# Optimization experiments

Hardware: AMD Instinct MI355X
Metric: run time of the kernel (lower is better)

## Reference

```python
import jax, jax.numpy as jnp
import numpy as np

NUM_USERS = 100000
NUM_ITEMS = 100000
EMBED_F = 64
BATCH = 8192
MAX_HIST = 200
MU = 3.5


def setup_inputs() -> dict:
    key = jax.random.key(0)
    ks = jax.random.split(key, 9)
    inv_f = 1.0 / EMBED_F
    return {
        "user": jax.random.randint(ks[0], (BATCH,), 0, NUM_USERS),
        "item": jax.random.randint(ks[1], (BATCH,), 0, NUM_ITEMS),
        "implicit": jax.random.randint(ks[2], (BATCH, MAX_HIST), 0, NUM_ITEMS),
        "hist_len": jax.random.randint(ks[3], (BATCH,), 0, MAX_HIST),
        "P": jax.random.normal(ks[4], (NUM_USERS, EMBED_F), dtype=jnp.float32) * inv_f,
        "Q": jax.random.normal(ks[5], (NUM_ITEMS, EMBED_F), dtype=jnp.float32) * inv_f,
        "Y": jax.random.normal(ks[6], (NUM_ITEMS, EMBED_F), dtype=jnp.float32) * inv_f,
        "bu": jax.random.normal(ks[7], (NUM_USERS,), dtype=jnp.float32),
        "bi": jax.random.normal(ks[8], (NUM_ITEMS,), dtype=jnp.float32),
    }


def reference(user, item, implicit, hist_len, P, Q, Y, bu, bi):
    # lengths clamped to >=1 (original assumes every user has implicit feedback)
    lengths = jnp.maximum(hist_len, 1)                      # [B]
    mask = (jnp.arange(MAX_HIST)[None, :] < lengths[:, None]).astype(P.dtype)  # [B,H]

    # baseline estimate: mu + b_u + b_i
    bui = MU + bu[user] + bi[item]                          # [B]

    P_u = P[user]                                           # [B,F]
    Q_i = Q[item]                                           # [B,F]

    # ragged embedding-bag sum over implicit items (masked gather+sum)
    Y_g = Y[implicit]                                       # [B,H,F]
    y_sum = jnp.einsum("bhf,bh->bf", Y_g, mask)             # [B,F]
    norm = lengths.astype(P.dtype) ** -0.5                  # [B]

    rui = bui + jnp.sum(P_u * (Q_i + norm[:, None] * y_sum), axis=1)
    return rui
```

## Files before the change

kernel.cpp:

```cpp
#include <hip/hip_runtime.h>

#define BATCH_SZ 8192
#define MAX_HIST 200
#define EMBED_F 64

__global__ __launch_bounds__(256) void svdpp_kernel(
    const int*   __restrict__ user,
    const int*   __restrict__ item,
    const int*   __restrict__ implicit,
    const int*   __restrict__ hist_len,
    const float* __restrict__ P,
    const float* __restrict__ Q,
    const float* __restrict__ Y,
    const float* __restrict__ bu,
    const float* __restrict__ bi,
    float*       __restrict__ out)
{
    const int wave_id = (int)((blockIdx.x * blockDim.x + threadIdx.x) >> 6);
    const int lane    = (int)(threadIdx.x & 63);
    if (wave_id >= BATCH_SZ) return;
    const int b = wave_id;

    const int L = max(hist_len[b], 1);
    const int* idx_row = implicit + (size_t)b * MAX_HIST;

    int4 my_idx = make_int4(0, 0, 0, 0);
    if (lane < MAX_HIST / 4)
        my_idx = *reinterpret_cast<const int4*>(idx_row + lane * 4);

    float acc = 0.0f;
    int h = 0;
    for (; h + 8 <= L; h += 8) {
        const int s0 = h >> 2, s1 = s0 + 1;
        const int i0 = __shfl(my_idx.x, s0, 64);
        const int i1 = __shfl(my_idx.y, s0, 64);
        const int i2 = __shfl(my_idx.z, s0, 64);
        const int i3 = __shfl(my_idx.w, s0, 64);
        const int i4 = __shfl(my_idx.x, s1, 64);
        const int i5 = __shfl(my_idx.y, s1, 64);
        const int i6 = __shfl(my_idx.z, s1, 64);
        const int i7 = __shfl(my_idx.w, s1, 64);
        const float y0 = Y[(size_t)i0 * EMBED_F + lane];
        const float y1 = Y[(size_t)i1 * EMBED_F + lane];
        const float y2 = Y[(size_t)i2 * EMBED_F + lane];
        const float y3 = Y[(size_t)i3 * EMBED_F + lane];
        const float y4 = Y[(size_t)i4 * EMBED_F + lane];
        const float y5 = Y[(size_t)i5 * EMBED_F + lane];
        const float y6 = Y[(size_t)i6 * EMBED_F + lane];
        const float y7 = Y[(size_t)i7 * EMBED_F + lane];
        acc += ((y0 + y1) + (y2 + y3)) + ((y4 + y5) + (y6 + y7));
    }
    for (; h < L; ++h) {
        const int s = h >> 2, c = h & 3;
        const int ix = __shfl(my_idx.x, s, 64);
        const int iy = __shfl(my_idx.y, s, 64);
        const int iz = __shfl(my_idx.z, s, 64);
        const int iw = __shfl(my_idx.w, s, 64);
        const int i  = (c == 0) ? ix : (c == 1) ? iy : (c == 2) ? iz : iw;
        acc += Y[(size_t)i * EMBED_F + lane];
    }

    const int u = user[b];
    const int it = item[b];
    const float pu = P[(size_t)u  * EMBED_F + lane];
    const float qi = Q[(size_t)it * EMBED_F + lane];
    const float norm = 1.0f / sqrtf((float)L);

    float v = pu * (qi + norm * acc);
    #pragma unroll
    for (int off = 32; off > 0; off >>= 1)
        v += __shfl_xor(v, off, 64);

    if (lane == 0)
        out[b] = 3.5f + bu[u] + bi[it] + v;
}

extern "C" void kernel_launch(void* const* d_in, const int* in_sizes, int n_in,
                              void* d_out, int out_size, void* d_ws, size_t ws_size,
                              hipStream_t stream) {
    const int*   user     = (const int*)  d_in[0];
    const int*   item     = (const int*)  d_in[1];
    const int*   implicit = (const int*)  d_in[2];
    const int*   hist_len = (const int*)  d_in[3];
    const float* P        = (const float*)d_in[4];
    const float* Q        = (const float*)d_in[5];
    const float* Y        = (const float*)d_in[6];
    const float* bu       = (const float*)d_in[7];
    const float* bi       = (const float*)d_in[8];
    float* out = (float*)d_out;

    const int threads = 256;
    const int blocks  = BATCH_SZ / 4;
    svdpp_kernel<<<blocks, threads, 0, stream>>>(
        user, item, implicit, hist_len, P, Q, Y, bu, bi, out);
}
```

Measured before the change: 140.5 us.

## Gather four embedding rows per wave with float4 loads and LDS-staged indices

Measured after the change: 138.9 us. Within noise of the previous version (-1.2%).

```diff
diff --git a/kernel.cpp b/kernel.cpp
--- a/kernel.cpp
+++ b/kernel.cpp
@@ -3,6 +3,10 @@
 #define BATCH_SZ 8192
 #define MAX_HIST 200
 #define EMBED_F 64
+
+__device__ __forceinline__ float4 f4add(float4 a, float4 b) {
+    return make_float4(a.x + b.x, a.y + b.y, a.z + b.z, a.w + b.w);
+}
 
 __global__ __launch_bounds__(256) void svdpp_kernel(
     const int*   __restrict__ user,
@@ -16,59 +20,87 @@
     const float* __restrict__ bi,
     float*       __restrict__ out)
 {
-    const int wave_id = (int)((blockIdx.x * blockDim.x + threadIdx.x) >> 6);
-    const int lane    = (int)(threadIdx.x & 63);
-    if (wave_id >= BATCH_SZ) return;
-    const int b = wave_id;
+    __shared__ int lds_idx[4][MAX_HIST];
+
+    const int wblk = (int)(threadIdx.x >> 6);
+    const int b    = (int)(blockIdx.x * 4 + wblk);
+    const int lane = (int)(threadIdx.x & 63);
+    const int g = lane >> 4;
+    const int s = lane & 15;
 
     const int L = max(hist_len[b], 1);
+
     const int* idx_row = implicit + (size_t)b * MAX_HIST;
+    if (lane < MAX_HIST / 4) {
+        int4 v = *reinterpret_cast<const int4*>(idx_row + lane * 4);
+        *reinterpret_cast<int4*>(&lds_idx[wblk][lane * 4]) = v;
+    }
+    __syncthreads();
 
-    int4 my_idx = make_int4(0, 0, 0, 0);
-    if (lane < MAX_HIST / 4)
-        my_idx = *reinterpret_cast<const int4*>(idx_row + lane * 4);
+    const int* myidx = lds_idx[wblk];
+    const float4* __restrict__ Y4 = reinterpret_cast<const float4*>(Y);
 
-    float acc = 0.0f;
+    float4 acc = make_float4(0.f, 0.f, 0.f, 0.f);
     int h = 0;
-    for (; h + 8 <= L; h += 8) {
-        const int s0 = h >> 2, s1 = s0 + 1;
-        const int i0 = __shfl(my_idx.x, s0, 64);
-        const int i1 = __shfl(my_idx.y, s0, 64);
-        const int i2 = __shfl(my_idx.z, s0, 64);
-        const int i3 = __shfl(my_idx.w, s0, 64);
-        const int i4 = __shfl(my_idx.x, s1, 64);
-        const int i5 = __shfl(my_idx.y, s1, 64);
-        const int i6 = __shfl(my_idx.z, s1, 64);
-        const int i7 = __shfl(my_idx.w, s1, 64);
-        const float y0 = Y[(size_t)i0 * EMBED_F + lane];
-        const float y1 = Y[(size_t)i1 * EMBED_F + lane];
-        const float y2 = Y[(size_t)i2 * EMBED_F + lane];
-        const float y3 = Y[(size_t)i3 * EMBED_F + lane];
-        const float y4 = Y[(size_t)i4 * EMBED_F + lane];
-        const float y5 = Y[(size_t)i5 * EMBED_F + lane];
-        const float y6 = Y[(size_t)i6 * EMBED_F + lane];
-        const float y7 = Y[(size_t)i7 * EMBED_F + lane];
-        acc += ((y0 + y1) + (y2 + y3)) + ((y4 + y5) + (y6 + y7));
+
+    for (; h + 32 <= L; h += 32) {
+        const int i0 = myidx[h      + g];
+        const int i1 = myidx[h + 4  + g];
+        const int i2 = myidx[h + 8  + g];
+        const int i3 = myidx[h + 12 + g];
+        const int i4 = myidx[h + 16 + g];
+        const int i5 = myidx[h + 20 + g];
+        const int i6 = myidx[h + 24 + g];
+        const int i7 = myidx[h + 28 + g];
+        const float4 y0 = Y4[(size_t)i0 * 16 + s];
+        const float4 y1 = Y4[(size_t)i1 * 16 + s];
+        const float4 y2 = Y4[(size_t)i2 * 16 + s];
+        const float4 y3 = Y4[(size_t)i3 * 16 + s];
+        const float4 y4 = Y4[(size_t)i4 * 16 + s];
+        const float4 y5 = Y4[(size_t)i5 * 16 + s];
+        const float4 y6 = Y4[(size_t)i6 * 16 + s];
+        const float4 y7 = Y4[(size_t)i7 * 16 + s];
+        acc = f4add(acc, f4add(f4add(f4add(y0, y1), f4add(y2, y3)),
+                               f4add(f4add(y4, y5), f4add(y6, y7))));
     }
-    for (; h < L; ++h) {
-        const int s = h >> 2, c = h & 3;
-        const int ix = __shfl(my_idx.x, s, 64);
-        const int iy = __shfl(my_idx.y, s, 64);
-        const int iz = __shfl(my_idx.z, s, 64);
-        const int iw = __shfl(my_idx.w, s, 64);
-        const int i  = (c == 0) ? ix : (c == 1) ? iy : (c == 2) ? iz : iw;
-        acc += Y[(size_t)i * EMBED_F + lane];
+    for (; h + 16 <= L; h += 16) {
+        const int i0 = myidx[h      + g];
+        const int i1 = myidx[h + 4  + g];
+        const int i2 = myidx[h + 8  + g];
+        const int i3 = myidx[h + 12 + g];
+        const float4 y0 = Y4[(size_t)i0 * 16 + s];
+        const float4 y1 = Y4[(size_t)i1 * 16 + s];
+        const float4 y2 = Y4[(size_t)i2 * 16 + s];
+        const float4 y3 = Y4[(size_t)i3 * 16 + s];
+        acc = f4add(acc, f4add(f4add(y0, y1), f4add(y2, y3)));
+    }
+    for (; h < L; h += 4) {
+        const int i = myidx[h + g];
+        const float4 y = Y4[(size_t)i * 16 + s];
+        if (h + g < L) acc = f4add(acc, y);
     }
 
-    const int u = user[b];
+    #pragma unroll
+    for (int off = 16; off < 64; off <<= 1) {
+        acc.x += __shfl_xor(acc.x, off, 64);
+        acc.y += __shfl_xor(acc.y, off, 64);
+        acc.z += __shfl_xor(acc.z, off, 64);
+        acc.w += __shfl_xor(acc.w, off, 64);
+    }
+
+    const int u  = user[b];
     const int it = item[b];
-    const float pu = P[(size_t)u  * EMBED_F + lane];
-    const float qi = Q[(size_t)it * EMBED_F + lane];
+    const float4 pu = reinterpret_cast<const float4*>(P)[(size_t)u  * 16 + s];
+    const float4 qi = reinterpret_cast<const float4*>(Q)[(size_t)it * 16 + s];
     const float norm = 1.0f / sqrtf((float)L);
 
-    float v = pu * (qi + norm * acc);
+    float v = pu.x * (qi.x + norm * acc.x)
+            + pu.y * (qi.y + norm * acc.y)
+            + pu.z * (qi.z + norm * acc.z)
+            + pu.w * (qi.w + norm * acc.w);
+
     #pragma unroll
-    for (int off = 32; off > 0; off >>= 1)
+    for (int off = 1; off < 16; off <<= 1)
         v += __shfl_xor(v, off, 64);
 
     if (lane == 0)
```
